# Kernel tuning notes

Measured on AMD Instinct MI355X. Metric: run time of the kernel, lower is better.

## Reference

```python
import jax, jax.numpy as jnp
import numpy as np

N_ATOMS = 100_000
N_PAIRS = 3_200_000
N_SPECIES = 8
BOX = 5.0


def _sym(key, lo, hi):
    m = jax.random.uniform(key, (N_SPECIES, N_SPECIES), minval=lo, maxval=hi, dtype=jnp.float32)
    return 0.5 * (m + m.T)  # species matrices must be symmetric


def setup_inputs() -> dict:
    key = jax.random.key(0)
    ks = jax.random.split(key, 7)
    positions = jax.random.uniform(ks[0], (N_ATOMS, 3), dtype=jnp.float32) * BOX
    cell = BOX * jnp.eye(3, dtype=jnp.float32)
    i = jax.random.randint(ks[1], (N_PAIRS,), 0, N_ATOMS)
    off = jax.random.randint(ks[2], (N_PAIRS,), 1, N_ATOMS)  # exclude self-pairs (r=0)
    j = (i + off) % N_ATOMS
    mapping = jnp.stack([i, j]).astype(jnp.int64)
    shifts = jnp.zeros((N_PAIRS, 3), dtype=jnp.float32)
    species = jax.random.randint(ks[3], (N_ATOMS,), 0, N_SPECIES).astype(jnp.int64)
    sigma_matrix = _sym(ks[4], 1.0, 2.0)
    epsilon_matrix = _sym(ks[5], 0.5, 1.5)
    alpha_matrix = _sym(ks[6], 2.0, 3.0)
    return dict(positions=positions, cell=cell, sigma_matrix=sigma_matrix,
                epsilon_matrix=epsilon_matrix, alpha_matrix=alpha_matrix,
                shifts=shifts, mapping=mapping, species=species)


def reference(positions, cell, sigma_matrix, epsilon_matrix, alpha_matrix, shifts, mapping, species):
    n = positions.shape[0]
    i, j = mapping[0], mapping[1]
    # pair displacements with periodic shifts: dr = r_j - r_i + S @ cell
    dr = positions[j] - positions[i] + shifts @ cell              # [P,3]
    r = jnp.sqrt(jnp.sum(dr * dr, axis=-1))                       # [P]
    # species-pair parameter lookup
    si, sj = species[i], species[j]
    sigma = sigma_matrix[si, sj]
    eps = epsilon_matrix[si, sj]
    alpha = alpha_matrix[si, sj]
    # soft-sphere pair energy: eps/alpha * (1 - r/sigma)^alpha for r < sigma, else 0
    mask = r < sigma
    base = jnp.where(mask, 1.0 - r / sigma, 1.0)                  # safe base for pow/grad
    e_pair = jnp.where(mask, (eps / alpha) * base ** alpha, 0.0)
    energy = 0.5 * jnp.sum(e_pair)
    energies = (jax.ops.segment_sum(0.5 * e_pair, i, num_segments=n)
                + jax.ops.segment_sum(0.5 * e_pair, j, num_segments=n))
    # pair force magnitude: -dE/dr = eps/sigma * (1 - r/sigma)^(alpha-1)
    f_pair = jnp.where(mask, (eps / sigma) * base ** (alpha - 1.0), 0.0)
    fvec = (f_pair / r)[:, None] * dr                             # [P,3]
    forces = (jax.ops.segment_sum(fvec, i, num_segments=n)
              - jax.ops.segment_sum(fvec, j, num_segments=n))
    # virial stress
    volume = jnp.abs(jnp.linalg.det(cell))
    stress = -jnp.einsum('pi,pj->ij', dr, fvec) / volume          # [3,3]
    return energy, energies, forces, stress
```

## Files before the change

kernel.cpp:

```cpp
#include <hip/hip_runtime.h>
#include <math.h>

#define NSP 8

typedef float v4f __attribute__((ext_vector_type(4)));

#define FSCALE 1048576.0f
#define FINV   (1.0f/1048576.0f)
#define ESCALE 131072.0f
#define EINV   (1.0f/131072.0f)
#define FBIAS  2.0f

__global__ __launch_bounds__(256) void init_kernel(
    const float* __restrict__ pos, const int* __restrict__ spec,
    v4f* __restrict__ ps, unsigned long long* __restrict__ accum, int n)
{
    int t = blockIdx.x * blockDim.x + threadIdx.x;
    if (t < n) {
        v4f v;
        v.x = pos[3 * t];
        v.y = pos[3 * t + 1];
        v.z = pos[3 * t + 2];
        v.w = __int_as_float(spec[t]);
        ps[t] = v;
        accum[2 * t]     = 0ULL;
        accum[2 * t + 1] = 0ULL;
    }
}

__global__ __launch_bounds__(256, 8) void pair_kernel(
    const v4f* __restrict__ ps,
    const float* __restrict__ cell,
    const float* __restrict__ sigma_m,
    const float* __restrict__ eps_m,
    const float* __restrict__ alpha_m,
    const float* __restrict__ shifts,
    const int* __restrict__ mapping,
    unsigned long long* __restrict__ accum,
    float* __restrict__ partials,
    int n_atoms, int n_pairs)
{
    __shared__ float s_sigma[64], s_invsig[64], s_alpha[64], s_eoa[64], s_eos[64];
    __shared__ float s_cell[9];
    const int t = threadIdx.x;
    if (t < 64) {
        float sg = sigma_m[t], ep = eps_m[t], al = alpha_m[t];
        s_sigma[t]  = sg;
        s_invsig[t] = 1.0f / sg;
        s_alpha[t]  = al;
        s_eoa[t]    = ep / al;
        s_eos[t]    = ep / sg;
    }
    if (t < 9) s_cell[t] = cell[t];
    __syncthreads();

    const int p = blockIdx.x * 256 + t;
    float le = 0.f, s00 = 0.f, s01 = 0.f, s02 = 0.f, s11 = 0.f, s12 = 0.f, s22 = 0.f;

    if (p < n_pairs) {
        const int i = mapping[p];
        const int j = mapping[p + n_pairs];
        const float shx = shifts[3 * p];
        const float shy = shifts[3 * p + 1];
        const float shz = shifts[3 * p + 2];

        const v4f pi = ps[i];
        const v4f pj = ps[j];

        const float drx = pj.x - pi.x + shx * s_cell[0] + shy * s_cell[3] + shz * s_cell[6];
        const float dry = pj.y - pi.y + shx * s_cell[1] + shy * s_cell[4] + shz * s_cell[7];
        const float drz = pj.z - pi.z + shx * s_cell[2] + shy * s_cell[5] + shz * s_cell[8];
        const float r = sqrtf(drx * drx + dry * dry + drz * drz);

        const int idx = __float_as_int(pi.w) * NSP + __float_as_int(pj.w);
        if (r < s_sigma[idx]) {
            const float base = 1.0f - r * s_invsig[idx];
            const float pb   = __powf(base, s_alpha[idx] - 1.0f);
            const float e    = s_eoa[idx] * pb * base;
            const float sc   = s_eos[idx] * pb / r;
            const float fx = sc * drx, fy = sc * dry, fz = sc * drz;

            le  = e;
            s00 = drx * fx; s01 = drx * fy; s02 = drx * fz;
            s11 = dry * fy; s12 = dry * fz; s22 = drz * fz;

            const float he = 0.5f * e;
            const unsigned long long he_fix = (unsigned long long)__float2uint_rn(he * ESCALE);
            {
                const unsigned long long fxq = (unsigned long long)__float2uint_rn((fx + FBIAS) * FSCALE);
                const unsigned long long fyq = (unsigned long long)__float2uint_rn((fy + FBIAS) * FSCALE);
                const unsigned long long fzq = (unsigned long long)__float2uint_rn((fz + FBIAS) * FSCALE);
                atomicAdd(&accum[2 * i],     (fxq << 32) | fyq);
                atomicAdd(&accum[2 * i + 1], (1ULL << 56) | (he_fix << 32) | fzq);
            }
            {
                const unsigned long long fxq = (unsigned long long)__float2uint_rn((FBIAS - fx) * FSCALE);
                const unsigned long long fyq = (unsigned long long)__float2uint_rn((FBIAS - fy) * FSCALE);
                const unsigned long long fzq = (unsigned long long)__float2uint_rn((FBIAS - fz) * FSCALE);
                atomicAdd(&accum[2 * j],     (fxq << 32) | fyq);
                atomicAdd(&accum[2 * j + 1], (1ULL << 56) | (he_fix << 32) | fzq);
            }
        }
    }

    float vals[7] = {le, s00, s01, s02, s11, s12, s22};
    #pragma unroll
    for (int k = 0; k < 7; ++k) {
        float v = vals[k];
        #pragma unroll
        for (int off = 32; off > 0; off >>= 1)
            v += __shfl_down(v, off, 64);
        vals[k] = v;
    }
    __shared__ float s_red[4][7];
    const int wave = t >> 6, lane = t & 63;
    if (lane == 0) {
        #pragma unroll
        for (int k = 0; k < 7; ++k) s_red[wave][k] = vals[k];
    }
    __syncthreads();
    if (t < 8) {
        float v = 0.f;
        if (t < 7) v = s_red[0][t] + s_red[1][t] + s_red[2][t] + s_red[3][t];
        partials[(size_t)blockIdx.x * 8 + t] = v;
    }
}

__global__ __launch_bounds__(256) void finalize_kernel(
    const unsigned long long* __restrict__ accum,
    const float* __restrict__ partials, int nblocks,
    const float* __restrict__ cell, float* __restrict__ out, int n_atoms)
{
    if (blockIdx.x == 0) {
        const int t = threadIdx.x;
        float a0 = 0.f, a1 = 0.f, a2 = 0.f, a3 = 0.f, a4 = 0.f, a5 = 0.f, a6 = 0.f;
        for (int b = t; b < nblocks; b += 256) {
            const v4f lo = *(const v4f*)(partials + (size_t)b * 8);
            const v4f hi = *(const v4f*)(partials + (size_t)b * 8 + 4);
            a0 += lo.x; a1 += lo.y; a2 += lo.z; a3 += lo.w;
            a4 += hi.x; a5 += hi.y; a6 += hi.z;
        }
        float vals[7] = {a0, a1, a2, a3, a4, a5, a6};
        #pragma unroll
        for (int k = 0; k < 7; ++k) {
            float v = vals[k];
            #pragma unroll
            for (int off = 32; off > 0; off >>= 1)
                v += __shfl_down(v, off, 64);
            vals[k] = v;
        }
        __shared__ float s_red[4][7];
        const int wave = t >> 6, lane = t & 63;
        if (lane == 0) {
            #pragma unroll
            for (int k = 0; k < 7; ++k) s_red[wave][k] = vals[k];
        }
        __syncthreads();
        if (t == 0) {
            float tot[7];
            #pragma unroll
            for (int k = 0; k < 7; ++k)
                tot[k] = s_red[0][k] + s_red[1][k] + s_red[2][k] + s_red[3][k];
            out[0] = 0.5f * tot[0];
            const float c0 = cell[0], c1 = cell[1], c2 = cell[2];
            const float c3 = cell[3], c4 = cell[4], c5 = cell[5];
            const float c6 = cell[6], c7 = cell[7], c8 = cell[8];
            const float det = c0 * (c4 * c8 - c5 * c7)
                            - c1 * (c3 * c8 - c5 * c6)
                            + c2 * (c3 * c7 - c4 * c6);
            const float nv = -1.0f / fabsf(det);
            float* st = out + 1 + 4 * n_atoms;
            st[0] = tot[1] * nv;  st[1] = tot[2] * nv;  st[2] = tot[3] * nv;
            st[3] = tot[2] * nv;  st[4] = tot[4] * nv;  st[5] = tot[5] * nv;
            st[6] = tot[3] * nv;  st[7] = tot[5] * nv;  st[8] = tot[6] * nv;
        }
    } else {
        const int t = (blockIdx.x - 1) * 256 + threadIdx.x;
        if (t < n_atoms) {
            const unsigned long long A = accum[2 * t];
            const unsigned long long B = accum[2 * t + 1];
            const float cntb = (float)(unsigned)(B >> 56) * FBIAS;
            const float fx = (float)(unsigned)(A >> 32)          * FINV - cntb;
            const float fy = (float)(unsigned)(A & 0xFFFFFFFFu)  * FINV - cntb;
            const float fz = (float)(unsigned)(B & 0xFFFFFFFFu)  * FINV - cntb;
            const float he = (float)(unsigned)((B >> 32) & 0xFFFFFFu) * EINV;
            out[1 + t] = he;
            float* forces = out + 1 + n_atoms;
            forces[3 * t]     = fx;
            forces[3 * t + 1] = fy;
            forces[3 * t + 2] = fz;
        }
    }
}

__global__ __launch_bounds__(256) void soft_sphere_fallback(
    const float* __restrict__ positions, const float* __restrict__ cell,
    const float* __restrict__ sigma_m, const float* __restrict__ eps_m,
    const float* __restrict__ alpha_m, const float* __restrict__ shifts,
    const int* __restrict__ mapping, const int* __restrict__ species,
    float* __restrict__ out, int n_atoms, int n_pairs)
{
    __shared__ float s_sigma[64], s_invsig[64], s_alpha[64], s_eoa[64], s_eos[64];
    __shared__ float s_cell[9];
    const int t = threadIdx.x;
    if (t < 64) {
        float sg = sigma_m[t], ep = eps_m[t], al = alpha_m[t];
        s_sigma[t] = sg; s_invsig[t] = 1.0f / sg; s_alpha[t] = al;
        s_eoa[t] = ep / al; s_eos[t] = ep / sg;
    }
    if (t < 9) s_cell[t] = cell[t];
    __syncthreads();

    float* energies = out + 1;
    float* forces   = out + 1 + n_atoms;
    float* stress   = out + 1 + 4 * n_atoms;

    float le = 0.f, s00 = 0.f, s01 = 0.f, s02 = 0.f, s11 = 0.f, s12 = 0.f, s22 = 0.f;
    const int stride = blockDim.x * gridDim.x;
    for (int p = blockIdx.x * blockDim.x + t; p < n_pairs; p += stride) {
        const int i = mapping[p], j = mapping[p + n_pairs];
        const float drx = positions[3*j]   - positions[3*i]   + shifts[3*p]*s_cell[0] + shifts[3*p+1]*s_cell[3] + shifts[3*p+2]*s_cell[6];
        const float dry = positions[3*j+1] - positions[3*i+1] + shifts[3*p]*s_cell[1] + shifts[3*p+1]*s_cell[4] + shifts[3*p+2]*s_cell[7];
        const float drz = positions[3*j+2] - positions[3*i+2] + shifts[3*p]*s_cell[2] + shifts[3*p+1]*s_cell[5] + shifts[3*p+2]*s_cell[8];
        const float r = sqrtf(drx*drx + dry*dry + drz*drz);
        const int idx = species[i] * NSP + species[j];
        if (r < s_sigma[idx]) {
            const float base = 1.0f - r * s_invsig[idx];
            const float pb = __powf(base, s_alpha[idx] - 1.0f);
            const float e = s_eoa[idx] * pb * base;
            const float sc = s_eos[idx] * pb / r;
            const float fx = sc*drx, fy = sc*dry, fz = sc*drz;
            le += e;
            s00 += drx*fx; s01 += drx*fy; s02 += drx*fz;
            s11 += dry*fy; s12 += dry*fz; s22 += drz*fz;
            atomicAdd(&energies[i], 0.5f*e); atomicAdd(&energies[j], 0.5f*e);
            atomicAdd(&forces[3*i], fx); atomicAdd(&forces[3*i+1], fy); atomicAdd(&forces[3*i+2], fz);
            atomicAdd(&forces[3*j], -fx); atomicAdd(&forces[3*j+1], -fy); atomicAdd(&forces[3*j+2], -fz);
        }
    }
    float vals[7] = {le, s00, s01, s02, s11, s12, s22};
    #pragma unroll
    for (int k = 0; k < 7; ++k) {
        float v = vals[k];
        #pragma unroll
        for (int off = 32; off > 0; off >>= 1) v += __shfl_down(v, off, 64);
        vals[k] = v;
    }
    __shared__ float s_red[4][7];
    const int wave = t >> 6, lane = t & 63;
    if (lane == 0) for (int k = 0; k < 7; ++k) s_red[wave][k] = vals[k];
    __syncthreads();
    if (t == 0) {
        const int nwaves = blockDim.x >> 6;
        float tot[7];
        for (int k = 0; k < 7; ++k) {
            float v = s_red[0][k];
            for (int w = 1; w < nwaves; ++w) v += s_red[w][k];
            tot[k] = v;
        }
        atomicAdd(&out[0], 0.5f * tot[0]);
        const float det = s_cell[0]*(s_cell[4]*s_cell[8]-s_cell[5]*s_cell[7])
                        - s_cell[1]*(s_cell[3]*s_cell[8]-s_cell[5]*s_cell[6])
                        + s_cell[2]*(s_cell[3]*s_cell[7]-s_cell[4]*s_cell[6]);
        const float nv = -1.0f / fabsf(det);
        atomicAdd(&stress[0], tot[1]*nv); atomicAdd(&stress[1], tot[2]*nv); atomicAdd(&stress[2], tot[3]*nv);
        atomicAdd(&stress[3], tot[2]*nv); atomicAdd(&stress[4], tot[4]*nv); atomicAdd(&stress[5], tot[5]*nv);
        atomicAdd(&stress[6], tot[3]*nv); atomicAdd(&stress[7], tot[5]*nv); atomicAdd(&stress[8], tot[6]*nv);
    }
}

extern "C" void kernel_launch(void* const* d_in, const int* in_sizes, int n_in,
                              void* d_out, int out_size, void* d_ws, size_t ws_size,
                              hipStream_t stream) {
    const float* positions = (const float*)d_in[0];
    const float* cell      = (const float*)d_in[1];
    const float* sigma_m   = (const float*)d_in[2];
    const float* eps_m     = (const float*)d_in[3];
    const float* alpha_m   = (const float*)d_in[4];
    const float* shifts    = (const float*)d_in[5];
    const int*   mapping   = (const int*)d_in[6];
    const int*   species   = (const int*)d_in[7];
    float* out = (float*)d_out;

    const int n_atoms = in_sizes[0] / 3;
    const int n_pairs = in_sizes[6] / 2;

    const int pk_blocks = (n_pairs + 255) / 256;
    const int rp_blocks = (n_atoms + 255) / 256;

    const size_t off_accum = 0;
    const size_t off_ps    = off_accum + (size_t)n_atoms * 16;
    const size_t off_part  = off_ps    + (size_t)n_atoms * 16;
    const size_t need      = off_part + (size_t)pk_blocks * 32;

    if (ws_size < need) {
        hipMemsetAsync(d_out, 0, (size_t)out_size * sizeof(float), stream);
        int blocks = ((n_pairs + 3) / 4 + 255) / 256;
        soft_sphere_fallback<<<blocks, 256, 0, stream>>>(
            positions, cell, sigma_m, eps_m, alpha_m, shifts, mapping, species,
            out, n_atoms, n_pairs);
        return;
    }

    char* wsb = (char*)d_ws;
    unsigned long long* accum    = (unsigned long long*)(wsb + off_accum);
    v4f*                ps       = (v4f*)(wsb + off_ps);
    float*              partials = (float*)(wsb + off_part);

    init_kernel<<<rp_blocks, 256, 0, stream>>>(positions, species, ps, accum, n_atoms);

    pair_kernel<<<pk_blocks, 256, 0, stream>>>(
        ps, cell, sigma_m, eps_m, alpha_m, shifts, mapping,
        accum, partials, n_atoms, n_pairs);

    finalize_kernel<<<1 + rp_blocks, 256, 0, stream>>>(
        accum, partials, pk_blocks, cell, out, n_atoms);
}
```

Baseline: 169.2 us.

## Compute energy and virial from per-atom sums instead of per-pair reductions

Removes the per-block energy and stress reductions from the pair kernel and derives total energy and the virial from per-atom accumulated energies and forces times positions in the finalize kernel. A correction term accumulated with atomics handles pairs with nonzero periodic shifts. This cuts shuffle reductions, the block barrier and partials writes from the hot pair loop. In exchange, the stress now depends on the fixed-point quantized forces, and finalize uses a grid-stride loop with global atomics on the output.

```diff
diff --git a/kernel.cpp b/kernel.cpp
--- a/kernel.cpp
+++ b/kernel.cpp
@@ -2,6 +2,7 @@
 #include <math.h>
 
 #define NSP 8
+#define FBLOCKS 64
 
 typedef float v4f __attribute__((ext_vector_type(4)));
 
@@ -13,10 +14,11 @@
 
 __global__ __launch_bounds__(256) void init_kernel(
     const float* __restrict__ pos, const int* __restrict__ spec,
-    v4f* __restrict__ ps, unsigned long long* __restrict__ accum, int n)
+    v4f* __restrict__ ps, unsigned long long* __restrict__ accum,
+    float* __restrict__ corr, float* __restrict__ out, int n_atoms)
 {
     int t = blockIdx.x * blockDim.x + threadIdx.x;
-    if (t < n) {
+    if (t < n_atoms) {
         v4f v;
         v.x = pos[3 * t];
         v.y = pos[3 * t + 1];
@@ -25,6 +27,11 @@
         ps[t] = v;
         accum[2 * t]     = 0ULL;
         accum[2 * t + 1] = 0ULL;
+    }
+    if (t == 0) out[0] = 0.f;
+    if (t < 9) {
+        out[1 + 4 * n_atoms + t] = 0.f;
+        corr[t] = 0.f;
     }
 }
 
@@ -37,7 +44,7 @@
     const float* __restrict__ shifts,
     const int* __restrict__ mapping,
     unsigned long long* __restrict__ accum,
-    float* __restrict__ partials,
+    float* __restrict__ corr,
     int n_atoms, int n_pairs)
 {
     __shared__ float s_sigma[64], s_invsig[64], s_alpha[64], s_eoa[64], s_eos[64];
@@ -55,55 +62,90 @@
     __syncthreads();
 
     const int p = blockIdx.x * 256 + t;
-    float le = 0.f, s00 = 0.f, s01 = 0.f, s02 = 0.f, s11 = 0.f, s12 = 0.f, s22 = 0.f;
-
-    if (p < n_pairs) {
-        const int i = mapping[p];
-        const int j = mapping[p + n_pairs];
-        const float shx = shifts[3 * p];
-        const float shy = shifts[3 * p + 1];
-        const float shz = shifts[3 * p + 2];
-
-        const v4f pi = ps[i];
-        const v4f pj = ps[j];
-
-        const float drx = pj.x - pi.x + shx * s_cell[0] + shy * s_cell[3] + shz * s_cell[6];
-        const float dry = pj.y - pi.y + shx * s_cell[1] + shy * s_cell[4] + shz * s_cell[7];
-        const float drz = pj.z - pi.z + shx * s_cell[2] + shy * s_cell[5] + shz * s_cell[8];
-        const float r = sqrtf(drx * drx + dry * dry + drz * drz);
-
-        const int idx = __float_as_int(pi.w) * NSP + __float_as_int(pj.w);
-        if (r < s_sigma[idx]) {
-            const float base = 1.0f - r * s_invsig[idx];
-            const float pb   = __powf(base, s_alpha[idx] - 1.0f);
-            const float e    = s_eoa[idx] * pb * base;
-            const float sc   = s_eos[idx] * pb / r;
-            const float fx = sc * drx, fy = sc * dry, fz = sc * drz;
-
-            le  = e;
-            s00 = drx * fx; s01 = drx * fy; s02 = drx * fz;
-            s11 = dry * fy; s12 = dry * fz; s22 = drz * fz;
-
-            const float he = 0.5f * e;
-            const unsigned long long he_fix = (unsigned long long)__float2uint_rn(he * ESCALE);
-            {
-                const unsigned long long fxq = (unsigned long long)__float2uint_rn((fx + FBIAS) * FSCALE);
-                const unsigned long long fyq = (unsigned long long)__float2uint_rn((fy + FBIAS) * FSCALE);
-                const unsigned long long fzq = (unsigned long long)__float2uint_rn((fz + FBIAS) * FSCALE);
-                atomicAdd(&accum[2 * i],     (fxq << 32) | fyq);
-                atomicAdd(&accum[2 * i + 1], (1ULL << 56) | (he_fix << 32) | fzq);
-            }
-            {
-                const unsigned long long fxq = (unsigned long long)__float2uint_rn((FBIAS - fx) * FSCALE);
-                const unsigned long long fyq = (unsigned long long)__float2uint_rn((FBIAS - fy) * FSCALE);
-                const unsigned long long fzq = (unsigned long long)__float2uint_rn((FBIAS - fz) * FSCALE);
-                atomicAdd(&accum[2 * j],     (fxq << 32) | fyq);
-                atomicAdd(&accum[2 * j + 1], (1ULL << 56) | (he_fix << 32) | fzq);
-            }
-        }
-    }
-
-    float vals[7] = {le, s00, s01, s02, s11, s12, s22};
+    if (p >= n_pairs) return;
+
+    const int i = mapping[p];
+    const int j = mapping[p + n_pairs];
+    const float shx = shifts[3 * p];
+    const float shy = shifts[3 * p + 1];
+    const float shz = shifts[3 * p + 2];
+
+    const v4f pi = ps[i];
+    const v4f pj = ps[j];
+
+    const float drx = pj.x - pi.x + shx * s_cell[0] + shy * s_cell[3] + shz * s_cell[6];
+    const float dry = pj.y - pi.y + shx * s_cell[1] + shy * s_cell[4] + shz * s_cell[7];
+    const float drz = pj.z - pi.z + shx * s_cell[2] + shy * s_cell[5] + shz * s_cell[8];
+    const float r = sqrtf(drx * drx + dry * dry + drz * drz);
+
+    const int idx = __float_as_int(pi.w) * NSP + __float_as_int(pj.w);
+    if (r < s_sigma[idx]) {
+        const float base = 1.0f - r * s_invsig[idx];
+        const float pb   = __powf(base, s_alpha[idx] - 1.0f);
+        const float e    = s_eoa[idx] * pb * base;
+        const float sc   = s_eos[idx] * pb / r;
+        const float fx = sc * drx, fy = sc * dry, fz = sc * drz;
+
+        const float he = 0.5f * e;
+        const unsigned long long he_fix = (unsigned long long)__float2uint_rn(he * ESCALE);
+        {
+            const unsigned long long fxq = (unsigned long long)__float2uint_rn((fx + FBIAS) * FSCALE);
+            const unsigned long long fyq = (unsigned long long)__float2uint_rn((fy + FBIAS) * FSCALE);
+            const unsigned long long fzq = (unsigned long long)__float2uint_rn((fz + FBIAS) * FSCALE);
+            atomicAdd(&accum[2 * i],     (fxq << 32) | fyq);
+            atomicAdd(&accum[2 * i + 1], (1ULL << 56) | (he_fix << 32) | fzq);
+        }
+        {
+            const unsigned long long fxq = (unsigned long long)__float2uint_rn((FBIAS - fx) * FSCALE);
+            const unsigned long long fyq = (unsigned long long)__float2uint_rn((FBIAS - fy) * FSCALE);
+            const unsigned long long fzq = (unsigned long long)__float2uint_rn((FBIAS - fz) * FSCALE);
+            atomicAdd(&accum[2 * j],     (fxq << 32) | fyq);
+            atomicAdd(&accum[2 * j + 1], (1ULL << 56) | (he_fix << 32) | fzq);
+        }
+
+        if (shx != 0.f || shy != 0.f || shz != 0.f) {
+            const float scx = shx * s_cell[0] + shy * s_cell[3] + shz * s_cell[6];
+            const float scy = shx * s_cell[1] + shy * s_cell[4] + shz * s_cell[7];
+            const float scz = shx * s_cell[2] + shy * s_cell[5] + shz * s_cell[8];
+            atomicAdd(&corr[0], scx * fx); atomicAdd(&corr[1], scx * fy); atomicAdd(&corr[2], scx * fz);
+            atomicAdd(&corr[3], scy * fx); atomicAdd(&corr[4], scy * fy); atomicAdd(&corr[5], scy * fz);
+            atomicAdd(&corr[6], scz * fx); atomicAdd(&corr[7], scz * fy); atomicAdd(&corr[8], scz * fz);
+        }
+    }
+}
+
+__global__ __launch_bounds__(256) void finalize_kernel(
+    const unsigned long long* __restrict__ accum,
+    const v4f* __restrict__ ps,
+    const float* __restrict__ corr,
+    const float* __restrict__ cell,
+    float* __restrict__ out, int n_atoms)
+{
+    const int t  = threadIdx.x;
+    const int gs = gridDim.x * 256;
+    float se = 0.f, s00 = 0.f, s01 = 0.f, s02 = 0.f, s11 = 0.f, s12 = 0.f, s22 = 0.f;
+    float* __restrict__ forces = out + 1 + n_atoms;
+
+    for (int a = blockIdx.x * 256 + t; a < n_atoms; a += gs) {
+        const unsigned long long A = accum[2 * a];
+        const unsigned long long B = accum[2 * a + 1];
+        const float cntb = (float)(unsigned)(B >> 56) * FBIAS;
+        const float fx = (float)(unsigned)(A >> 32)          * FINV - cntb;
+        const float fy = (float)(unsigned)(A & 0xFFFFFFFFu)  * FINV - cntb;
+        const float fz = (float)(unsigned)(B & 0xFFFFFFFFu)  * FINV - cntb;
+        const float he = (float)(unsigned)((B >> 32) & 0xFFFFFFu) * EINV;
+        out[1 + a] = he;
+        forces[3 * a]     = fx;
+        forces[3 * a + 1] = fy;
+        forces[3 * a + 2] = fz;
+
+        const v4f pa = ps[a];
+        se  += he;
+        s00 += pa.x * fx; s01 += pa.x * fy; s02 += pa.x * fz;
+        s11 += pa.y * fy; s12 += pa.y * fz; s22 += pa.z * fz;
+    }
+
+    float vals[7] = {se, s00, s01, s02, s11, s12, s22};
     #pragma unroll
     for (int k = 0; k < 7; ++k) {
         float v = vals[k];
@@ -119,76 +161,29 @@
         for (int k = 0; k < 7; ++k) s_red[wave][k] = vals[k];
     }
     __syncthreads();
-    if (t < 8) {
-        float v = 0.f;
-        if (t < 7) v = s_red[0][t] + s_red[1][t] + s_red[2][t] + s_red[3][t];
-        partials[(size_t)blockIdx.x * 8 + t] = v;
-    }
-}
-
-__global__ __launch_bounds__(256) void finalize_kernel(
-    const unsigned long long* __restrict__ accum,
-    const float* __restrict__ partials, int nblocks,
-    const float* __restrict__ cell, float* __restrict__ out, int n_atoms)
-{
-    if (blockIdx.x == 0) {
-        const int t = threadIdx.x;
-        float a0 = 0.f, a1 = 0.f, a2 = 0.f, a3 = 0.f, a4 = 0.f, a5 = 0.f, a6 = 0.f;
-        for (int b = t; b < nblocks; b += 256) {
-            const v4f lo = *(const v4f*)(partials + (size_t)b * 8);
-            const v4f hi = *(const v4f*)(partials + (size_t)b * 8 + 4);
-            a0 += lo.x; a1 += lo.y; a2 += lo.z; a3 += lo.w;
-            a4 += hi.x; a5 += hi.y; a6 += hi.z;
-        }
-        float vals[7] = {a0, a1, a2, a3, a4, a5, a6};
+    if (t == 0) {
+        float tot[7];
         #pragma unroll
-        for (int k = 0; k < 7; ++k) {
-            float v = vals[k];
+        for (int k = 0; k < 7; ++k)
+            tot[k] = s_red[0][k] + s_red[1][k] + s_red[2][k] + s_red[3][k];
+
+        const float c0 = cell[0], c1 = cell[1], c2 = cell[2];
+        const float c3 = cell[3], c4 = cell[4], c5 = cell[5];
+        const float c6 = cell[6], c7 = cell[7], c8 = cell[8];
+        const float det = c0 * (c4 * c8 - c5 * c7)
+                        - c1 * (c3 * c8 - c5 * c6)
+                        + c2 * (c3 * c7 - c4 * c6);
+        const float inv = 1.0f / fabsf(det);
+
+        atomicAdd(&out[0], 0.5f * tot[0]);
+        float* st = out + 1 + 4 * n_atoms;
+        atomicAdd(&st[0], tot[1] * inv);  atomicAdd(&st[1], tot[2] * inv);  atomicAdd(&st[2], tot[3] * inv);
+        atomicAdd(&st[3], tot[2] * inv);  atomicAdd(&st[4], tot[4] * inv);  atomicAdd(&st[5], tot[5] * inv);
+        atomicAdd(&st[6], tot[3] * inv);  atomicAdd(&st[7], tot[5] * inv);  atomicAdd(&st[8], tot[6] * inv);
+
+        if (blockIdx.x == 0) {
             #pragma unroll
-            for (int off = 32; off > 0; off >>= 1)
-                v += __shfl_down(v, off, 64);
-            vals[k] = v;
-        }
-        __shared__ float s_red[4][7];
-        const int wave = t >> 6, lane = t & 63;
-        if (lane == 0) {
-            #pragma unroll
-            for (int k = 0; k < 7; ++k) s_red[wave][k] = vals[k];
-        }
-        __syncthreads();
-        if (t == 0) {
-            float tot[7];
-            #pragma unroll
-            for (int k = 0; k < 7; ++k)
-                tot[k] = s_red[0][k] + s_red[1][k] + s_red[2][k] + s_red[3][k];
-            out[0] = 0.5f * tot[0];
-            const float c0 = cell[0], c1 = cell[1], c2 = cell[2];
-            const float c3 = cell[3], c4 = cell[4], c5 = cell[5];
-            const float c6 = cell[6], c7 = cell[7], c8 = cell[8];
-            const float det = c0 * (c4 * c8 - c5 * c7)
-                            - c1 * (c3 * c8 - c5 * c6)
-                            + c2 * (c3 * c7 - c4 * c6);
-            const float nv = -1.0f / fabsf(det);
-            float* st = out + 1 + 4 * n_atoms;
-            st[0] = tot[1] * nv;  st[1] = tot[2] * nv;  st[2] = tot[3] * nv;
-            st[3] = tot[2] * nv;  st[4] = tot[4] * nv;  st[5] = tot[5] * nv;
-            st[6] = tot[3] * nv;  st[7] = tot[5] * nv;  st[8] = tot[6] * nv;
-        }
-    } else {
-        const int t = (blockIdx.x - 1) * 256 + threadIdx.x;
-        if (t < n_atoms) {
-            const unsigned long long A = accum[2 * t];
-            const unsigned long long B = accum[2 * t + 1];
-            const float cntb = (float)(unsigned)(B >> 56) * FBIAS;
-            const float fx = (float)(unsigned)(A >> 32)          * FINV - cntb;
-            const float fy = (float)(unsigned)(A & 0xFFFFFFFFu)  * FINV - cntb;
-            const float fz = (float)(unsigned)(B & 0xFFFFFFFFu)  * FINV - cntb;
-            const float he = (float)(unsigned)((B >> 32) & 0xFFFFFFu) * EINV;
-            out[1 + t] = he;
-            float* forces = out + 1 + n_atoms;
-            forces[3 * t]     = fx;
-            forces[3 * t + 1] = fy;
-            forces[3 * t + 2] = fz;
+            for (int k = 0; k < 9; ++k) atomicAdd(&st[k], -corr[k] * inv);
         }
     }
 }
@@ -290,8 +285,8 @@
 
     const size_t off_accum = 0;
     const size_t off_ps    = off_accum + (size_t)n_atoms * 16;
-    const size_t off_part  = off_ps    + (size_t)n_atoms * 16;
-    const size_t need      = off_part + (size_t)pk_blocks * 32;
+    const size_t off_corr  = off_ps    + (size_t)n_atoms * 16;
+    const size_t need      = off_corr + 128;
 
     if (ws_size < need) {
         hipMemsetAsync(d_out, 0, (size_t)out_size * sizeof(float), stream);
@@ -303,16 +298,17 @@
     }
 
     char* wsb = (char*)d_ws;
-    unsigned long long* accum    = (unsigned long long*)(wsb + off_accum);
-    v4f*                ps       = (v4f*)(wsb + off_ps);
-    float*              partials = (float*)(wsb + off_part);
-
-    init_kernel<<<rp_blocks, 256, 0, stream>>>(positions, species, ps, accum, n_atoms);
+    unsigned long long* accum = (unsigned long long*)(wsb + off_accum);
+    v4f*                ps    = (v4f*)(wsb + off_ps);
+    float*              corr  = (float*)(wsb + off_corr);
+
+    init_kernel<<<rp_blocks, 256, 0, stream>>>(
+        positions, species, ps, accum, corr, out, n_atoms);
 
     pair_kernel<<<pk_blocks, 256, 0, stream>>>(
         ps, cell, sigma_m, eps_m, alpha_m, shifts, mapping,
-        accum, partials, n_atoms, n_pairs);
-
-    finalize_kernel<<<1 + rp_blocks, 256, 0, stream>>>(
-        accum, partials, pk_blocks, cell, out, n_atoms);
-}
+        accum, corr, n_atoms, n_pairs);
+
+    finalize_kernel<<<FBLOCKS, 256, 0, stream>>>(
+        accum, ps, corr, cell, out, n_atoms);
+}
```

Result: faster. 163.2 us (-3.5%).
